# Performance work log

Measured on AMD Instinct MI355X. Metric: run time of the kernel, lower is better.

Reference implementation:

```python
import jax, jax.numpy as jnp
import numpy as np

N = 20000      # total nodes across the mini-batch of graphs
E = 320000     # edges (avg degree 16)
B = 16         # graphs in the batch
HEADS = 8
EPS_BN = 1e-5
NEG_SLOPE = 0.2


def _lin(k, fan_in, fan_out):
    return (jax.random.normal(k, (fan_in, fan_out), jnp.float32) / np.float32(np.sqrt(fan_in)))


def setup_inputs() -> dict:
    key = jax.random.key(0)
    ks = jax.random.split(key, 24)
    inp = {}
    inp["x"] = jax.random.normal(ks[0], (N, 3), jnp.float32)
    inp["edge_index"] = jax.random.randint(ks[1], (2, E), 0, N, dtype=jnp.int32)
    inp["batch"] = jnp.sort(jax.random.randint(ks[2], (N,), 0, B, dtype=jnp.int32))
    # GATConv params: lin weight [in, heads*out], att_src/att_dst [heads,out], bias [heads*out]
    dims = [(3, 16), (128, 32), (256, 64)]
    for i, (cin, cout) in enumerate(dims, start=1):
        base = 3 + 5 * i
        inp[f"W{i}"] = _lin(ks[base], cin, HEADS * cout)
        inp[f"as{i}"] = jax.random.normal(ks[base + 1], (HEADS, cout), jnp.float32) * 0.1
        inp[f"ad{i}"] = jax.random.normal(ks[base + 2], (HEADS, cout), jnp.float32) * 0.1
        inp[f"b{i}"] = jnp.zeros((HEADS * cout,), jnp.float32)
        inp[f"g{i}"] = jnp.ones((HEADS * cout,), jnp.float32)
        inp[f"be{i}"] = jnp.zeros((HEADS * cout,), jnp.float32)
    inp["fcW"] = _lin(ks[20], 512, 10)
    inp["fcb"] = jnp.zeros((10,), jnp.float32)
    return inp


def gat_layer(x, src, dst, W, a_s, a_d, bias, heads, out_ch):
    n = x.shape[0]
    h = (x @ W).reshape(n, heads, out_ch)              # [N,H,C]
    al_s = jnp.einsum('nhc,hc->nh', h, a_s)            # [N,H]
    al_d = jnp.einsum('nhc,hc->nh', h, a_d)
    e = jax.nn.leaky_relu(al_s[src] + al_d[dst], NEG_SLOPE)   # [E,H]
    m = jax.ops.segment_max(e, dst, num_segments=n)    # per-dst softmax (stable)
    e = jnp.exp(e - m[dst])
    denom = jax.ops.segment_sum(e, dst, num_segments=n)
    alpha = e / (denom[dst] + 1e-16)
    out = jax.ops.segment_sum(h[src] * alpha[:, :, None], dst, num_segments=n)
    return out.reshape(n, heads * out_ch) + bias


def bn_relu(x, g, b):
    mu = x.mean(0)
    var = x.var(0)  # biased, as torch BN uses for normalization
    return jax.nn.relu((x - mu) * jax.lax.rsqrt(var + EPS_BN) * g + b)


def reference(x, edge_index, batch, W1, as1, ad1, b1, g1, be1,
              W2, as2, ad2, b2, g2, be2, W3, as3, ad3, b3, g3, be3, fcW, fcb):
    n = x.shape[0]
    loops = jnp.arange(n, dtype=edge_index.dtype)
    src = jnp.concatenate([edge_index[0], loops])  # add_self_loops=True (PyG default)
    dst = jnp.concatenate([edge_index[1], loops])
    h = bn_relu(gat_layer(x, src, dst, W1, as1, ad1, b1, HEADS, 16), g1, be1)
    h = bn_relu(gat_layer(h, src, dst, W2, as2, ad2, b2, HEADS, 32), g2, be2)
    h = bn_relu(gat_layer(h, src, dst, W3, as3, ad3, b3, HEADS, 64), g3, be3)
    pooled = jax.ops.segment_max(h, batch, num_segments=B)  # global_max_pool
    return pooled @ fcW + fcb
```

## Files before the change

kernel.cpp:

```cpp
#include <hip/hip_runtime.h>
#include <hip/hip_bf16.h>

#define HEADS 8
#define EPS_BN 1e-5f
#define NEG_SLOPE 0.2f
#define BN_NB 256

typedef __attribute__((ext_vector_type(8))) short bf16x8;
typedef __attribute__((ext_vector_type(4))) float f32x4;

__device__ __forceinline__ float bf2f(unsigned short u) {
    return __uint_as_float(((unsigned int)u) << 16);
}

__device__ __forceinline__ unsigned short f2bf(float f) {
    __hip_bfloat16 b = __float2bfloat16(f);
    return *reinterpret_cast<unsigned short*>(&b);
}

__device__ __forceinline__ void gld_lds16(const ushort* g, ushort* l) {
    __builtin_amdgcn_global_load_lds(
        (const __attribute__((address_space(1))) unsigned int*)g,
        (__attribute__((address_space(3))) unsigned int*)l, 16, 0, 0);
}


__global__ void count_kernel(const int* __restrict__ ei, int E, int N, int* __restrict__ counts) {
    int i = blockIdx.x * blockDim.x + threadIdx.x;
    int total = E + N;
    if (i >= total) return;
    int d = (i < E) ? ei[E + i] : (i - E);
    atomicAdd(&counts[d], 1);
}

__global__ __launch_bounds__(1024) void scan_block_kernel(const int* __restrict__ counts,
                                                          int* __restrict__ offs,
                                                          int* __restrict__ part, int n) {
    __shared__ int tile[1024];
    int tid = threadIdx.x;
    int gid = blockIdx.x * 1024 + tid;
    int v = (gid < n) ? counts[gid] : 0;
    tile[tid] = v;
    __syncthreads();
    for (int off = 1; off < 1024; off <<= 1) {
        int t = (tid >= off) ? tile[tid - off] : 0;
        __syncthreads();
        tile[tid] += t;
        __syncthreads();
    }
    if (gid < n) offs[gid + 1] = tile[tid];
    if (tid == 1023) part[blockIdx.x] = tile[1023];
}

__global__ __launch_bounds__(1024) void scan_add_kernel(int* __restrict__ offs,
                                                        const int* __restrict__ part, int n) {
    __shared__ int base;
    if (threadIdx.x == 0) {
        int s = 0;
        for (int i = 0; i < (int)blockIdx.x; ++i) s += part[i];
        base = s;
    }
    __syncthreads();
    int gid = blockIdx.x * 1024 + threadIdx.x;
    if (gid < n) offs[gid + 1] += base;
    if (gid == 0) offs[0] = 0;
}

__global__ void scatter_kernel(const int* __restrict__ ei, int E, int N,
                               const int* __restrict__ offs, int* __restrict__ cursor,
                               int* __restrict__ csr_src) {
    int i = blockIdx.x * blockDim.x + threadIdx.x;
    int total = E + N;
    if (i >= total) return;
    int s, d;
    if (i < E) { s = ei[i]; d = ei[E + i]; } else { s = i - E; d = i - E; }
    int slot = atomicAdd(&cursor[d], 1);
    csr_src[offs[d] + slot] = s;
}


__global__ __launch_bounds__(256) void linear1_al_tr_kernel(const float* __restrict__ x,
                                                            const float* __restrict__ W,
                                                            const float* __restrict__ a_s,
                                                            const float* __restrict__ a_d,
                                                            ushort* __restrict__ h,
                                                            float* __restrict__ als,
                                                            float* __restrict__ ald, int N,
                                                            const float* __restrict__ W2,
                                                            ushort* __restrict__ Wt2,
                                                            const float* __restrict__ W3,
                                                            ushort* __restrict__ Wt3) {
    __shared__ float t[32][33];
    int tid = threadIdx.x;
    int bid = blockIdx.x;
    if (bid < 160) {
        const float* Ws; ushort* Wt; int K, Nc, b;
        if (bid < 32) { Ws = W2; Wt = Wt2; K = 128; Nc = 256; b = bid; }
        else          { Ws = W3; Wt = Wt3; K = 256; Nc = 512; b = bid - 32; }
        int nb = Nc / 32;
        int bx = b % nb, by = b / nb;
        int n0 = bx * 32, k0 = by * 32;
        int lx = tid & 31, ly = tid >> 5;
        for (int r = ly; r < 32; r += 8) t[r][lx] = Ws[(size_t)(k0 + r) * Nc + n0 + lx];
        __syncthreads();
        for (int r = ly; r < 32; r += 8) Wt[(size_t)(n0 + r) * K + k0 + lx] = f2bf(t[lx][r]);
    }
    int n = bid * 2 + (tid >> 7);
    int f = tid & 127;
    if (n >= N) return;
    float acc = x[n * 3 + 0] * W[f] + x[n * 3 + 1] * W[128 + f] + x[n * 3 + 2] * W[256 + f];
    h[(size_t)n * 128 + f] = f2bf(acc);
    float s = acc * a_s[f];
    float ds = acc * a_d[f];
    s += __shfl_xor(s, 1);  ds += __shfl_xor(ds, 1);
    s += __shfl_xor(s, 2);  ds += __shfl_xor(ds, 2);
    s += __shfl_xor(s, 4);  ds += __shfl_xor(ds, 4);
    s += __shfl_xor(s, 8);  ds += __shfl_xor(ds, 8);
    if ((f & 15) == 0) {
        int head = f >> 4;
        als[n * 8 + head] = s;
        ald[n * 8 + head] = ds;
    }
}


template<int K, int C>
__global__ __launch_bounds__(256) void mfma_gemm_kernel(const ushort* __restrict__ A,
                                                        const float* __restrict__ scale,
                                                        const float* __restrict__ shift,
                                                        const ushort* __restrict__ Bt,
                                                        ushort* __restrict__ Cout,
                                                        const float* __restrict__ a_s,
                                                        const float* __restrict__ a_d,
                                                        float* __restrict__ als,
                                                        float* __restrict__ ald,
                                                        int M, int Ncols) {
    __shared__ __align__(16) ushort lA[128 * 64];
    __shared__ __align__(16) ushort lB[128 * 64];
    __shared__ __align__(16) float s_scale[K];
    __shared__ __align__(16) float s_shift[K];
    int tid = threadIdx.x;
    int l = tid & 63, w = tid >> 6;
    int m0 = blockIdx.x * 128;
    int n0 = blockIdx.y * 128;
    int wm = w >> 1, wn = w & 1;
    for (int i = tid; i < K; i += 256) {
        s_scale[i] = scale[i];
        s_shift[i] = shift[i];
    }
    f32x4 zero = {0.f, 0.f, 0.f, 0.f};
    f32x4 acc[4][4];
#pragma unroll
    for (int m = 0; m < 4; ++m)
#pragma unroll
        for (int n = 0; n < 4; ++n) acc[m][n] = zero;
    __syncthreads();

#pragma unroll
    for (int k0 = 0; k0 < K; k0 += 64) {
        if (k0) __syncthreads();
#pragma unroll
        for (int i = 0; i < 4; ++i) {
            int idx = (w * 4 + i) * 64 + l;
            int row = idx >> 3, p = idx & 7;
            int gc = (p ^ (row & 7)) * 8;
            gld_lds16(Bt + (size_t)(n0 + row) * K + k0 + gc, &lB[idx * 8]);
        }
#pragma unroll
        for (int i = 0; i < 4; ++i) {
            int idx = (w * 4 + i) * 64 + l;
            int row = idx >> 3, p = idx & 7;
            int gc = (p ^ (row & 7)) * 8;
            int ar = m0 + row; ar = (ar < M) ? ar : (M - 1);
            int kk = k0 + gc;
            uint4 raw = *(const uint4*)(A + (size_t)ar * K + kk);
            float4 sc0 = *(const float4*)(s_scale + kk);
            float4 sc1 = *(const float4*)(s_scale + kk + 4);
            float4 sh0 = *(const float4*)(s_shift + kk);
            float4 sh1 = *(const float4*)(s_shift + kk + 4);
            unsigned int rr0 = raw.x, rr1 = raw.y, rr2 = raw.z, rr3 = raw.w;
            float v0, v1;
            unsigned int o0, o1, o2, o3;
            v0 = fmaxf(__uint_as_float(rr0 << 16) * sc0.x + sh0.x, 0.f);
            v1 = fmaxf(__uint_as_float(rr0 & 0xffff0000u) * sc0.y + sh0.y, 0.f);
            o0 = (unsigned int)f2bf(v0) | ((unsigned int)f2bf(v1) << 16);
            v0 = fmaxf(__uint_as_float(rr1 << 16) * sc0.z + sh0.z, 0.f);
            v1 = fmaxf(__uint_as_float(rr1 & 0xffff0000u) * sc0.w + sh0.w, 0.f);
            o1 = (unsigned int)f2bf(v0) | ((unsigned int)f2bf(v1) << 16);
            v0 = fmaxf(__uint_as_float(rr2 << 16) * sc1.x + sh1.x, 0.f);
            v1 = fmaxf(__uint_as_float(rr2 & 0xffff0000u) * sc1.y + sh1.y, 0.f);
            o2 = (unsigned int)f2bf(v0) | ((unsigned int)f2bf(v1) << 16);
            v0 = fmaxf(__uint_as_float(rr3 << 16) * sc1.z + sh1.z, 0.f);
            v1 = fmaxf(__uint_as_float(rr3 & 0xffff0000u) * sc1.w + sh1.w, 0.f);
            o3 = (unsigned int)f2bf(v0) | ((unsigned int)f2bf(v1) << 16);
            uint4 pk = {o0, o1, o2, o3};
            *(uint4*)&lA[idx * 8] = pk;
        }
        __syncthreads();
#pragma unroll
        for (int ks = 0; ks < 2; ++ks) {
            bf16x8 af[4], bfr[4];
#pragma unroll
            for (int m = 0; m < 4; ++m) {
                int row = wm * 64 + m * 16 + (l & 15);
                int cp = (ks * 4 + (l >> 4)) ^ (row & 7);
                af[m] = *(const bf16x8*)&lA[row * 64 + cp * 8];
            }
#pragma unroll
            for (int n = 0; n < 4; ++n) {
                int row = wn * 64 + n * 16 + (l & 15);
                int cp = (ks * 4 + (l >> 4)) ^ (row & 7);
                bfr[n] = *(const bf16x8*)&lB[row * 64 + cp * 8];
            }
#pragma unroll
            for (int m = 0; m < 4; ++m)
#pragma unroll
                for (int n = 0; n < 4; ++n)
                    acc[m][n] = __builtin_amdgcn_mfma_f32_16x16x32_bf16(af[m], bfr[n], acc[m][n], 0, 0, 0);
        }
    }
    int lr = (l >> 4) * 4, lc = l & 15;
#pragma unroll
    for (int m = 0; m < 4; ++m) {
#pragma unroll
        for (int q = 0; q < 4; ++q) {
            int r = m0 + wm * 64 + m * 16 + lr + q;
            if (r < M) {
#pragma unroll
                for (int n = 0; n < 4; ++n) {
                    int c = n0 + wn * 64 + n * 16 + lc;
                    Cout[(size_t)r * Ncols + c] = f2bf(acc[m][n][q]);
                }
            }
        }
    }
    constexpr int GRP = (C == 64) ? 4 : 2;
    constexpr int NGRP = 4 / GRP;
    float asv[4], adv[4];
#pragma unroll
    for (int n = 0; n < 4; ++n) {
        int cc = n0 + wn * 64 + n * 16 + lc;
        asv[n] = a_s[cc];
        adv[n] = a_d[cc];
    }
#pragma unroll
    for (int m = 0; m < 4; ++m) {
#pragma unroll
        for (int q = 0; q < 4; ++q) {
            int r = m0 + wm * 64 + m * 16 + lr + q;
#pragma unroll
            for (int gg = 0; gg < NGRP; ++gg) {
                float s = 0.f, ds = 0.f;
#pragma unroll
                for (int nn = 0; nn < GRP; ++nn) {
                    int n = gg * GRP + nn;
                    s += acc[m][n][q] * asv[n];
                    ds += acc[m][n][q] * adv[n];
                }
                s += __shfl_xor(s, 1);  ds += __shfl_xor(ds, 1);
                s += __shfl_xor(s, 2);  ds += __shfl_xor(ds, 2);
                s += __shfl_xor(s, 4);  ds += __shfl_xor(ds, 4);
                s += __shfl_xor(s, 8);  ds += __shfl_xor(ds, 8);
                if (lc == 0 && r < M) {
                    int head = (n0 + wn * 64 + gg * (GRP * 16)) / C;
                    als[r * 8 + head] = s;
                    ald[r * 8 + head] = ds;
                }
            }
        }
    }
}


template<int CPL>
__device__ __forceinline__ void gather_accum(const ushort* hp, float wt, float* acc) {
    unsigned int u[CPL / 2];
    if constexpr (CPL == 8) {
        uint4 v = *(const uint4*)hp; u[0] = v.x; u[1] = v.y; u[2] = v.z; u[3] = v.w;
    } else if constexpr (CPL == 4) {
        uint2 v = *(const uint2*)hp; u[0] = v.x; u[1] = v.y;
    } else {
        u[0] = *(const unsigned int*)hp;
    }
#pragma unroll
    for (int j = 0; j < CPL / 2; ++j) {
        acc[2 * j]     += wt * __uint_as_float(u[j] << 16);
        acc[2 * j + 1] += wt * __uint_as_float(u[j] & 0xffff0000u);
    }
}

template<int F, int C>
__global__ __launch_bounds__(256) void aggregate_kernel(const ushort* __restrict__ h,
                                                        const float* __restrict__ als,
                                                        const float* __restrict__ ald,
                                                        const int* __restrict__ offs,
                                                        const int* __restrict__ csr_src,
                                                        const float* __restrict__ bias,
                                                        ushort* __restrict__ outbf, int N) {
    constexpr int CPL = F / 64;
    int w = threadIdx.x >> 6, l = threadIdx.x & 63;
    int d = blockIdx.x * 4 + w;
    if (d >= N) return;
    int start = offs[d];
    int deg = offs[d + 1] - start;
    int hf = l >> 3;
    int hw = l & 7;
    int jslot = l >> 3;
    float aldw = ald[d * 8 + hw];

    float acc[CPL];
#pragma unroll
    for (int j = 0; j < CPL; ++j) acc[j] = 0.f;
    float dsum = 0.f;
    float mrun = -1e30f;

    int nfull = deg & ~7;
    for (int eb = 0; eb < nfull; eb += 8) {
        int sE = (l < 8) ? csr_src[start + eb + l] : 0;
        int smy = __shfl(sE, jslot);
        float v = als[smy * 8 + hw] + aldw;
        v = (v > 0.f) ? v : NEG_SLOPE * v;
        float bm = v;
        bm = fmaxf(bm, __shfl_xor(bm, 8));
        bm = fmaxf(bm, __shfl_xor(bm, 16));
        bm = fmaxf(bm, __shfl_xor(bm, 32));
        float mnew = fmaxf(mrun, bm);
        float rs = __expf(mrun - mnew);
        float pw = __expf(v - mnew);
        dsum = dsum * rs + pw;
        float rsg = __shfl(rs, hf);
#pragma unroll
        for (int j = 0; j < CPL; ++j) acc[j] *= rsg;
        mrun = mnew;
#pragma unroll
        for (int j = 0; j < 8; ++j) {
            int sj = __shfl(sE, j);
            float wt = __shfl(pw, (j << 3) + hf);
            gather_accum<CPL>(h + (size_t)sj * F + l * CPL, wt, acc);
        }
    }
    int rem = deg - nfull;
    if (rem) {
        int sE = (l < rem) ? csr_src[start + nfull + l] : 0;
        int smy = __shfl(sE, jslot);
        float v = -1e30f;
        if (jslot < rem) {
            v = als[smy * 8 + hw] + aldw;
            v = (v > 0.f) ? v : NEG_SLOPE * v;
        }
        float bm = v;
        bm = fmaxf(bm, __shfl_xor(bm, 8));
        bm = fmaxf(bm, __shfl_xor(bm, 16));
        bm = fmaxf(bm, __shfl_xor(bm, 32));
        float mnew = fmaxf(mrun, bm);
        float rs = __expf(mrun - mnew);
        float pw = __expf(v - mnew);
        dsum = dsum * rs + pw;
        float rsg = __shfl(rs, hf);
#pragma unroll
        for (int j = 0; j < CPL; ++j) acc[j] *= rsg;
        for (int j = 0; j < rem; ++j) {
            int sj = __shfl(sE, j);
            float wt = __shfl(pw, (j << 3) + hf);
            gather_accum<CPL>(h + (size_t)sj * F + l * CPL, wt, acc);
        }
    }
    dsum += __shfl_xor(dsum, 8);
    dsum += __shfl_xor(dsum, 16);
    dsum += __shfl_xor(dsum, 32);
    float den = __shfl(dsum, hf);
    float inv = 1.0f / (den + 1e-16f);
    int cbase = l * CPL;
#pragma unroll
    for (int j = 0; j < CPL; ++j)
        outbf[(size_t)d * F + cbase + j] = f2bf(acc[j] * inv + bias[cbase + j]);
}


template<int F>
__global__ __launch_bounds__(256) void bnA_kernel(const ushort* __restrict__ xb,
                                                  float* __restrict__ part,
                                                  int N, int npb) {
    constexpr int F4 = F / 4;
    constexpr int RPI = 256 / F4;
    __shared__ float sdata[256 * 8];
    int tid = threadIdx.x;
    int c4 = tid % F4;
    int ro = tid / F4;
    int n0 = blockIdx.x * npb;
    int n1 = n0 + npb;
    if (n1 > N) n1 = N;
    float s0 = 0, s1 = 0, s2 = 0, s3 = 0, q0 = 0, q1 = 0, q2 = 0, q3 = 0;
    for (int r = n0 + ro; r < n1; r += RPI) {
        ushort4 u = *(const ushort4*)(xb + (size_t)r * F + c4 * 4);
        float v0 = bf2f(u.x), v1 = bf2f(u.y), v2 = bf2f(u.z), v3 = bf2f(u.w);
        s0 += v0; s1 += v1; s2 += v2; s3 += v3;
        q0 += v0 * v0; q1 += v1 * v1; q2 += v2 * v2; q3 += v3 * v3;
    }
    float* sp = &sdata[tid * 8];
    sp[0] = s0; sp[1] = s1; sp[2] = s2; sp[3] = s3;
    sp[4] = q0; sp[5] = q1; sp[6] = q2; sp[7] = q3;
    __syncthreads();
    if (tid < F4) {
        float t[8];
#pragma unroll
        for (int k = 0; k < 8; ++k) t[k] = sdata[tid * 8 + k];
        for (int j = 1; j < RPI; ++j) {
            const float* op = &sdata[(j * F4 + tid) * 8];
#pragma unroll
            for (int k = 0; k < 8; ++k) t[k] += op[k];
        }
        float* pb = part + (size_t)blockIdx.x * 2 * F;
#pragma unroll
        for (int k = 0; k < 4; ++k) {
            pb[tid * 4 + k]     = t[k];
            pb[F + tid * 4 + k] = t[4 + k];
        }
    }
}

template<int F>
__global__ void bnB_kernel(const float* __restrict__ part,
                           const float* __restrict__ g, const float* __restrict__ be,
                           float* __restrict__ scale, float* __restrict__ shift, int N) {
    int f = blockIdx.x * blockDim.x + threadIdx.x;
    if (f >= F) return;
    float sum = 0.f, sq = 0.f;
#pragma unroll 4
    for (int j = 0; j < BN_NB; ++j) {
        sum += part[(size_t)j * 2 * F + f];
        sq  += part[(size_t)j * 2 * F + F + f];
    }
    float invN = 1.0f / (float)N;
    float mean = sum * invN;
    float var = sq * invN - mean * mean;
    float sc = g[f] * rsqrtf(var + EPS_BN);
    scale[f] = sc;
    shift[f] = be[f] - mean * sc;
}


__global__ __launch_bounds__(256) void poolA_kernel(const ushort* __restrict__ xb,
                                                    const int* __restrict__ batch,
                                                    const float* __restrict__ scale,
                                                    const float* __restrict__ shift,
                                                    float* __restrict__ pooled8, int N) {
    int tid = threadIdx.x;
    int c4 = tid & 127;
    int ro = tid >> 7;
    int n0 = blockIdx.x * 64;
    int n1 = n0 + 64;
    if (n1 > N) n1 = N;
    float4 sc = ((const float4*)scale)[c4];
    float4 sh = ((const float4*)shift)[c4];
    float* pbase = pooled8 + (size_t)(blockIdx.x & 7) * (16 * 512);
    float m0 = 0.f, m1 = 0.f, m2 = 0.f, m3 = 0.f;
    int cur = -1;
    for (int n = n0 + ro; n < n1; n += 2) {
        int b = batch[n];
        if (b != cur) {
            if (cur >= 0) {
                int base = cur * 512 + c4 * 4;
                atomicMax((int*)&pbase[base],     __float_as_int(m0));
                atomicMax((int*)&pbase[base + 1], __float_as_int(m1));
                atomicMax((int*)&pbase[base + 2], __float_as_int(m2));
                atomicMax((int*)&pbase[base + 3], __float_as_int(m3));
            }
            cur = b;
            m0 = m1 = m2 = m3 = 0.f;
        }
        ushort4 u = *(const ushort4*)(xb + (size_t)n * 512 + c4 * 4);
        m0 = fmaxf(m0, bf2f(u.x) * sc.x + sh.x);
        m1 = fmaxf(m1, bf2f(u.y) * sc.y + sh.y);
        m2 = fmaxf(m2, bf2f(u.z) * sc.z + sh.z);
        m3 = fmaxf(m3, bf2f(u.w) * sc.w + sh.w);
    }
    if (cur >= 0) {
        int base = cur * 512 + c4 * 4;
        atomicMax((int*)&pbase[base],     __float_as_int(m0));
        atomicMax((int*)&pbase[base + 1], __float_as_int(m1));
        atomicMax((int*)&pbase[base + 2], __float_as_int(m2));
        atomicMax((int*)&pbase[base + 3], __float_as_int(m3));
    }
}

__global__ __launch_bounds__(512) void poolFC_kernel(const float* __restrict__ pooled8,
                                                     const float* __restrict__ fcW,
                                                     const float* __restrict__ fcb,
                                                     float* __restrict__ out) {
    __shared__ float sp[16 * 513];
    __shared__ float sw[512 * 10];
    int tid = threadIdx.x;
    for (int c = tid; c < 16 * 512; c += 512) {
        float m = pooled8[c];
#pragma unroll
        for (int k = 1; k < 8; ++k) m = fmaxf(m, pooled8[k * 16 * 512 + c]);
        int b = c >> 9, f = c & 511;
        sp[b * 513 + f] = m;
    }
    for (int i = tid; i < 512 * 10; i += 512) sw[i] = fcW[i];
    __syncthreads();
    if (tid < 160) {
        int b = tid / 10, j = tid % 10;
        float acc = fcb[j];
        const float* spb = &sp[b * 513];
#pragma unroll 8
        for (int f = 0; f < 512; ++f) acc += spb[f] * sw[f * 10 + j];
        out[tid] = acc;
    }
}


extern "C" void kernel_launch(void* const* d_in, const int* in_sizes, int n_in,
                              void* d_out, int out_size, void* d_ws, size_t ws_size,
                              hipStream_t stream) {
    const float* x   = (const float*)d_in[0];
    const int* ei    = (const int*)d_in[1];
    const int* batch = (const int*)d_in[2];
    const float* W1  = (const float*)d_in[3];
    const float* as1 = (const float*)d_in[4];
    const float* ad1 = (const float*)d_in[5];
    const float* b1  = (const float*)d_in[6];
    const float* g1  = (const float*)d_in[7];
    const float* be1 = (const float*)d_in[8];
    const float* W2  = (const float*)d_in[9];
    const float* as2 = (const float*)d_in[10];
    const float* ad2 = (const float*)d_in[11];
    const float* b2  = (const float*)d_in[12];
    const float* g2  = (const float*)d_in[13];
    const float* be2 = (const float*)d_in[14];
    const float* W3  = (const float*)d_in[15];
    const float* as3 = (const float*)d_in[16];
    const float* ad3 = (const float*)d_in[17];
    const float* b3  = (const float*)d_in[18];
    const float* g3  = (const float*)d_in[19];
    const float* be3 = (const float*)d_in[20];
    const float* fcW = (const float*)d_in[21];
    const float* fcb = (const float*)d_in[22];
    float* out = (float*)d_out;

    int N = in_sizes[0] / 3;
    int E = in_sizes[1] / 2;

    char* p = (char*)d_ws;
    auto alloc = [&](size_t bytes) {
        char* r = p;
        p += (bytes + 255) & ~(size_t)255;
        return r;
    };
    char* zbase   = p;
    int*   counts = (int*)alloc((size_t)N * 4);
    int*   cursor = (int*)alloc((size_t)N * 4);
    float* pooled8 = (float*)alloc(8 * 16 * 512 * 4);
    size_t zbytes = (size_t)(p - zbase);
    int*   offs   = (int*)alloc((size_t)(N + 1) * 4);
    int*   part   = (int*)alloc(64 * 4);
    int*   csr    = (int*)alloc((size_t)(E + N) * 4);
    ushort* h     = (ushort*)alloc((size_t)N * 512 * 2);
    ushort* aggbf = (ushort*)alloc((size_t)N * 512 * 2);
    ushort* Wt2   = (ushort*)alloc(256 * 128 * 2);
    ushort* Wt3   = (ushort*)alloc(512 * 256 * 2);
    float* als    = (float*)alloc((size_t)N * 8 * 4);
    float* ald    = (float*)alloc((size_t)N * 8 * 4);
    float* bnpart = (float*)alloc((size_t)BN_NB * 1024 * 4);
    float* scale  = (float*)alloc(512 * 4);
    float* shift  = (float*)alloc(512 * 4);

    int total_e = E + N;
    int nchunks = (N + 1023) / 1024;
    int mtiles = (N + 127) / 128;
    int bnnpb = (N + BN_NB - 1) / BN_NB;
    int ablocks = (N + 3) / 4;
    int pblocks = (N + 63) / 64;

    hipMemsetAsync(zbase, 0, zbytes, stream);

    count_kernel<<<(total_e + 255) / 256, 256, 0, stream>>>(ei, E, N, counts);
    scan_block_kernel<<<nchunks, 1024, 0, stream>>>(counts, offs, part, N);
    scan_add_kernel<<<nchunks, 1024, 0, stream>>>(offs, part, N);
    scatter_kernel<<<(total_e + 255) / 256, 256, 0, stream>>>(ei, E, N, offs, cursor, csr);

    linear1_al_tr_kernel<<<(N + 1) / 2, 256, 0, stream>>>(x, W1, as1, ad1, h, als, ald, N,
                                                          W2, Wt2, W3, Wt3);
    aggregate_kernel<128, 16><<<ablocks, 256, 0, stream>>>(h, als, ald, offs, csr, b1, aggbf, N);
    bnA_kernel<128><<<BN_NB, 256, 0, stream>>>(aggbf, bnpart, N, bnnpb);
    bnB_kernel<128><<<1, 128, 0, stream>>>(bnpart, g1, be1, scale, shift, N);

    mfma_gemm_kernel<128, 32><<<dim3(mtiles, 2), 256, 0, stream>>>(
        aggbf, scale, shift, Wt2, h, as2, ad2, als, ald, N, 256);
    aggregate_kernel<256, 32><<<ablocks, 256, 0, stream>>>(h, als, ald, offs, csr, b2, aggbf, N);
    bnA_kernel<256><<<BN_NB, 256, 0, stream>>>(aggbf, bnpart, N, bnnpb);
    bnB_kernel<256><<<1, 256, 0, stream>>>(bnpart, g2, be2, scale, shift, N);

    mfma_gemm_kernel<256, 64><<<dim3(mtiles, 4), 256, 0, stream>>>(
        aggbf, scale, shift, Wt3, h, as3, ad3, als, ald, N, 512);
    aggregate_kernel<512, 64><<<ablocks, 256, 0, stream>>>(h, als, ald, offs, csr, b3, aggbf, N);
    bnA_kernel<512><<<BN_NB, 256, 0, stream>>>(aggbf, bnpart, N, bnnpb);
    bnB_kernel<512><<<2, 256, 0, stream>>>(bnpart, g3, be3, scale, shift, N);

    poolA_kernel<<<pblocks, 256, 0, stream>>>(aggbf, batch, scale, shift, pooled8, N);
    poolFC_kernel<<<1, 512, 0, stream>>>(pooled8, fcW, fcb, out);
}
```

Measured before the change: 318.6 us.

## Fuse BN statistics into GAT aggregation epilogue and parallelize BN finalize

The separate bnA pass that re-read the aggregated bf16 features is removed. Its per-feature sum and sum-of-squares are now accumulated in shared memory inside the aggregate kernel, which grows to 8 warps per block, and written out as per-block partials. bnB is rewritten to reduce the roughly 2500 partials across several blocks, each using 8 row-groups. This saves a full read of the activations per layer, but adds LDS atomics in the epilogue and a much larger partial buffer that bnB must read.

Measured after the change: 658.0 us. 107% more time.

```diff
diff --git a/kernel.cpp b/kernel.cpp
--- a/kernel.cpp
+++ b/kernel.cpp
@@ -4,7 +4,6 @@
 #define HEADS 8
 #define EPS_BN 1e-5f
 #define NEG_SLOPE 0.2f
-#define BN_NB 256
 
 typedef __attribute__((ext_vector_type(8))) short bf16x8;
 typedef __attribute__((ext_vector_type(4))) float f32x4;
@@ -290,153 +289,142 @@
 }
 
 template<int F, int C>
-__global__ __launch_bounds__(256) void aggregate_kernel(const ushort* __restrict__ h,
+__global__ __launch_bounds__(512) void aggregate_kernel(const ushort* __restrict__ h,
                                                         const float* __restrict__ als,
                                                         const float* __restrict__ ald,
                                                         const int* __restrict__ offs,
                                                         const int* __restrict__ csr_src,
                                                         const float* __restrict__ bias,
-                                                        ushort* __restrict__ outbf, int N) {
+                                                        ushort* __restrict__ outbf,
+                                                        float* __restrict__ bnpart, int N) {
     constexpr int CPL = F / 64;
-    int w = threadIdx.x >> 6, l = threadIdx.x & 63;
-    int d = blockIdx.x * 4 + w;
-    if (d >= N) return;
-    int start = offs[d];
-    int deg = offs[d + 1] - start;
-    int hf = l >> 3;
-    int hw = l & 7;
-    int jslot = l >> 3;
-    float aldw = ald[d * 8 + hw];
-
-    float acc[CPL];
-#pragma unroll
-    for (int j = 0; j < CPL; ++j) acc[j] = 0.f;
-    float dsum = 0.f;
-    float mrun = -1e30f;
-
-    int nfull = deg & ~7;
-    for (int eb = 0; eb < nfull; eb += 8) {
-        int sE = (l < 8) ? csr_src[start + eb + l] : 0;
-        int smy = __shfl(sE, jslot);
-        float v = als[smy * 8 + hw] + aldw;
-        v = (v > 0.f) ? v : NEG_SLOPE * v;
-        float bm = v;
-        bm = fmaxf(bm, __shfl_xor(bm, 8));
-        bm = fmaxf(bm, __shfl_xor(bm, 16));
-        bm = fmaxf(bm, __shfl_xor(bm, 32));
-        float mnew = fmaxf(mrun, bm);
-        float rs = __expf(mrun - mnew);
-        float pw = __expf(v - mnew);
-        dsum = dsum * rs + pw;
-        float rsg = __shfl(rs, hf);
-#pragma unroll
-        for (int j = 0; j < CPL; ++j) acc[j] *= rsg;
-        mrun = mnew;
-#pragma unroll
-        for (int j = 0; j < 8; ++j) {
-            int sj = __shfl(sE, j);
-            float wt = __shfl(pw, (j << 3) + hf);
-            gather_accum<CPL>(h + (size_t)sj * F + l * CPL, wt, acc);
-        }
-    }
-    int rem = deg - nfull;
-    if (rem) {
-        int sE = (l < rem) ? csr_src[start + nfull + l] : 0;
-        int smy = __shfl(sE, jslot);
-        float v = -1e30f;
-        if (jslot < rem) {
-            v = als[smy * 8 + hw] + aldw;
+    __shared__ float sstat[2 * F];
+    int tid = threadIdx.x;
+    int w = tid >> 6, l = tid & 63;
+    int d = blockIdx.x * 8 + w;
+    for (int i = tid; i < 2 * F; i += 512) sstat[i] = 0.f;
+    __syncthreads();
+
+    if (d < N) {
+        int start = offs[d];
+        int deg = offs[d + 1] - start;
+        int hf = l >> 3;
+        int hw = l & 7;
+        int jslot = l >> 3;
+        float aldw = ald[d * 8 + hw];
+
+        float acc[CPL];
+#pragma unroll
+        for (int j = 0; j < CPL; ++j) acc[j] = 0.f;
+        float dsum = 0.f;
+        float mrun = -1e30f;
+
+        int nfull = deg & ~7;
+        for (int eb = 0; eb < nfull; eb += 8) {
+            int sE = (l < 8) ? csr_src[start + eb + l] : 0;
+            int smy = __shfl(sE, jslot);
+            float v = als[smy * 8 + hw] + aldw;
             v = (v > 0.f) ? v : NEG_SLOPE * v;
-        }
-        float bm = v;
-        bm = fmaxf(bm, __shfl_xor(bm, 8));
-        bm = fmaxf(bm, __shfl_xor(bm, 16));
-        bm = fmaxf(bm, __shfl_xor(bm, 32));
-        float mnew = fmaxf(mrun, bm);
-        float rs = __expf(mrun - mnew);
-        float pw = __expf(v - mnew);
-        dsum = dsum * rs + pw;
-        float rsg = __shfl(rs, hf);
-#pragma unroll
-        for (int j = 0; j < CPL; ++j) acc[j] *= rsg;
-        for (int j = 0; j < rem; ++j) {
-            int sj = __shfl(sE, j);
-            float wt = __shfl(pw, (j << 3) + hf);
-            gather_accum<CPL>(h + (size_t)sj * F + l * CPL, wt, acc);
-        }
-    }
-    dsum += __shfl_xor(dsum, 8);
-    dsum += __shfl_xor(dsum, 16);
-    dsum += __shfl_xor(dsum, 32);
-    float den = __shfl(dsum, hf);
-    float inv = 1.0f / (den + 1e-16f);
-    int cbase = l * CPL;
-#pragma unroll
-    for (int j = 0; j < CPL; ++j)
-        outbf[(size_t)d * F + cbase + j] = f2bf(acc[j] * inv + bias[cbase + j]);
+            float bm = v;
+            bm = fmaxf(bm, __shfl_xor(bm, 8));
+            bm = fmaxf(bm, __shfl_xor(bm, 16));
+            bm = fmaxf(bm, __shfl_xor(bm, 32));
+            float mnew = fmaxf(mrun, bm);
+            float rs = __expf(mrun - mnew);
+            float pw = __expf(v - mnew);
+            dsum = dsum * rs + pw;
+            float rsg = __shfl(rs, hf);
+#pragma unroll
+            for (int j = 0; j < CPL; ++j) acc[j] *= rsg;
+            mrun = mnew;
+#pragma unroll
+            for (int j = 0; j < 8; ++j) {
+                int sj = __shfl(sE, j);
+                float wt = __shfl(pw, (j << 3) + hf);
+                gather_accum<CPL>(h + (size_t)sj * F + l * CPL, wt, acc);
+            }
+        }
+        int rem = deg - nfull;
+        if (rem) {
+            int sE = (l < rem) ? csr_src[start + nfull + l] : 0;
+            int smy = __shfl(sE, jslot);
+            float v = -1e30f;
+            if (jslot < rem) {
+                v = als[smy * 8 + hw] + aldw;
+                v = (v > 0.f) ? v : NEG_SLOPE * v;
+            }
+            float bm = v;
+            bm = fmaxf(bm, __shfl_xor(bm, 8));
+            bm = fmaxf(bm, __shfl_xor(bm, 16));
+            bm = fmaxf(bm, __shfl_xor(bm, 32));
+            float mnew = fmaxf(mrun, bm);
+            float rs = __expf(mrun - mnew);
+            float pw = __expf(v - mnew);
+            dsum = dsum * rs + pw;
+            float rsg = __shfl(rs, hf);
+#pragma unroll
+            for (int j = 0; j < CPL; ++j) acc[j] *= rsg;
+            for (int j = 0; j < rem; ++j) {
+                int sj = __shfl(sE, j);
+                float wt = __shfl(pw, (j << 3) + hf);
+                gather_accum<CPL>(h + (size_t)sj * F + l * CPL, wt, acc);
+            }
+        }
+        dsum += __shfl_xor(dsum, 8);
+        dsum += __shfl_xor(dsum, 16);
+        dsum += __shfl_xor(dsum, 32);
+        float den = __shfl(dsum, hf);
+        float inv = 1.0f / (den + 1e-16f);
+        int cbase = l * CPL;
+#pragma unroll
+        for (int j = 0; j < CPL; ++j) {
+            unsigned short ob = f2bf(acc[j] * inv + bias[cbase + j]);
+            outbf[(size_t)d * F + cbase + j] = ob;
+            float vv = bf2f(ob);
+            atomicAdd(&sstat[cbase + j], vv);
+            atomicAdd(&sstat[F + cbase + j], vv * vv);
+        }
+    }
+    __syncthreads();
+    float* pb = bnpart + (size_t)blockIdx.x * 2 * F;
+    for (int i = tid; i < 2 * F; i += 512) pb[i] = sstat[i];
 }
 
 
 template<int F>
-__global__ __launch_bounds__(256) void bnA_kernel(const ushort* __restrict__ xb,
-                                                  float* __restrict__ part,
-                                                  int N, int npb) {
-    constexpr int F4 = F / 4;
-    constexpr int RPI = 256 / F4;
-    __shared__ float sdata[256 * 8];
-    int tid = threadIdx.x;
-    int c4 = tid % F4;
-    int ro = tid / F4;
-    int n0 = blockIdx.x * npb;
-    int n1 = n0 + npb;
-    if (n1 > N) n1 = N;
-    float s0 = 0, s1 = 0, s2 = 0, s3 = 0, q0 = 0, q1 = 0, q2 = 0, q3 = 0;
-    for (int r = n0 + ro; r < n1; r += RPI) {
-        ushort4 u = *(const ushort4*)(xb + (size_t)r * F + c4 * 4);
-        float v0 = bf2f(u.x), v1 = bf2f(u.y), v2 = bf2f(u.z), v3 = bf2f(u.w);
-        s0 += v0; s1 += v1; s2 += v2; s3 += v3;
-        q0 += v0 * v0; q1 += v1 * v1; q2 += v2 * v2; q3 += v3 * v3;
-    }
-    float* sp = &sdata[tid * 8];
-    sp[0] = s0; sp[1] = s1; sp[2] = s2; sp[3] = s3;
-    sp[4] = q0; sp[5] = q1; sp[6] = q2; sp[7] = q3;
-    __syncthreads();
-    if (tid < F4) {
-        float t[8];
-#pragma unroll
-        for (int k = 0; k < 8; ++k) t[k] = sdata[tid * 8 + k];
-        for (int j = 1; j < RPI; ++j) {
-            const float* op = &sdata[(j * F4 + tid) * 8];
-#pragma unroll
-            for (int k = 0; k < 8; ++k) t[k] += op[k];
-        }
-        float* pb = part + (size_t)blockIdx.x * 2 * F;
-#pragma unroll
-        for (int k = 0; k < 4; ++k) {
-            pb[tid * 4 + k]     = t[k];
-            pb[F + tid * 4 + k] = t[4 + k];
-        }
-    }
-}
-
-template<int F>
-__global__ void bnB_kernel(const float* __restrict__ part,
-                           const float* __restrict__ g, const float* __restrict__ be,
-                           float* __restrict__ scale, float* __restrict__ shift, int N) {
-    int f = blockIdx.x * blockDim.x + threadIdx.x;
-    if (f >= F) return;
-    float sum = 0.f, sq = 0.f;
-#pragma unroll 4
-    for (int j = 0; j < BN_NB; ++j) {
-        sum += part[(size_t)j * 2 * F + f];
-        sq  += part[(size_t)j * 2 * F + F + f];
-    }
-    float invN = 1.0f / (float)N;
-    float mean = sum * invN;
-    float var = sq * invN - mean * mean;
-    float sc = g[f] * rsqrtf(var + EPS_BN);
-    scale[f] = sc;
-    shift[f] = be[f] - mean * sc;
+__global__ __launch_bounds__(256) void bnB_kernel(const float* __restrict__ part,
+                                                  const float* __restrict__ g,
+                                                  const float* __restrict__ be,
+                                                  float* __restrict__ scale,
+                                                  float* __restrict__ shift,
+                                                  int N, int nb) {
+    __shared__ float sd[8][2][33];
+    int fl = threadIdx.x & 31;
+    int bc = threadIdx.x >> 5;
+    int f = blockIdx.x * 32 + fl;
+    int per = (nb + 7) / 8;
+    int b0 = bc * per;
+    int b1 = b0 + per; if (b1 > nb) b1 = nb;
+    float s = 0.f, q = 0.f;
+    for (int b = b0; b < b1; ++b) {
+        s += part[(size_t)b * 2 * F + f];
+        q += part[(size_t)b * 2 * F + F + f];
+    }
+    sd[bc][0][fl] = s;
+    sd[bc][1][fl] = q;
+    __syncthreads();
+    if (threadIdx.x < 32) {
+        float ss = 0.f, qq = 0.f;
+#pragma unroll
+        for (int k = 0; k < 8; ++k) { ss += sd[k][0][threadIdx.x]; qq += sd[k][1][threadIdx.x]; }
+        int fo = blockIdx.x * 32 + threadIdx.x;
+        float invN = 1.0f / (float)N;
+        float mean = ss * invN;
+        float var = qq * invN - mean * mean;
+        float sc = g[fo] * rsqrtf(var + EPS_BN);
+        scale[fo] = sc;
+        shift[fo] = be[fo] - mean * sc;
+    }
 }
 
 
@@ -562,15 +550,14 @@
     ushort* Wt3   = (ushort*)alloc(512 * 256 * 2);
     float* als    = (float*)alloc((size_t)N * 8 * 4);
     float* ald    = (float*)alloc((size_t)N * 8 * 4);
-    float* bnpart = (float*)alloc((size_t)BN_NB * 1024 * 4);
+    int ablocks   = (N + 7) / 8;
+    float* bnpart = (float*)alloc((size_t)ablocks * 2 * 512 * 4);
     float* scale  = (float*)alloc(512 * 4);
     float* shift  = (float*)alloc(512 * 4);
 
     int total_e = E + N;
     int nchunks = (N + 1023) / 1024;
     int mtiles = (N + 127) / 128;
-    int bnnpb = (N + BN_NB - 1) / BN_NB;
-    int ablocks = (N + 3) / 4;
     int pblocks = (N + 63) / 64;
 
     hipMemsetAsync(zbase, 0, zbytes, stream);
@@ -582,21 +569,21 @@
 
     linear1_al_tr_kernel<<<(N + 1) / 2, 256, 0, stream>>>(x, W1, as1, ad1, h, als, ald, N,
                                                           W2, Wt2, W3, Wt3);
-    aggregate_kernel<128, 16><<<ablocks, 256, 0, stream>>>(h, als, ald, offs, csr, b1, aggbf, N);
-    bnA_kernel<128><<<BN_NB, 256, 0, stream>>>(aggbf, bnpart, N, bnnpb);
-    bnB_kernel<128><<<1, 128, 0, stream>>>(bnpart, g1, be1, scale, shift, N);
+    aggregate_kernel<128, 16><<<ablocks, 512, 0, stream>>>(h, als, ald, offs, csr, b1,
+                                                           aggbf, bnpart, N);
+    bnB_kernel<128><<<4, 256, 0, stream>>>(bnpart, g1, be1, scale, shift, N, ablocks);
 
     mfma_gemm_kernel<128, 32><<<dim3(mtiles, 2), 256, 0, stream>>>(
         aggbf, scale, shift, Wt2, h, as2, ad2, als, ald, N, 256);
-    aggregate_kernel<256, 32><<<ablocks, 256, 0, stream>>>(h, als, ald, offs, csr, b2, aggbf, N);
-    bnA_kernel<256><<<BN_NB, 256, 0, stream>>>(aggbf, bnpart, N, bnnpb);
-    bnB_kernel<256><<<1, 256, 0, stream>>>(bnpart, g2, be2, scale, shift, N);
+    aggregate_kernel<256, 32><<<ablocks, 512, 0, stream>>>(h, als, ald, offs, csr, b2,
+                                                           aggbf, bnpart, N);
+    bnB_kernel<256><<<8, 256, 0, stream>>>(bnpart, g2, be2, scale, shift, N, ablocks);
 
     mfma_gemm_kernel<256, 64><<<dim3(mtiles, 4), 256, 0, stream>>>(
         aggbf, scale, shift, Wt3, h, as3, ad3, als, ald, N, 512);
-    aggregate_kernel<512, 64><<<ablocks, 256, 0, stream>>>(h, als, ald, offs, csr, b3, aggbf, N);
-    bnA_kernel<512><<<BN_NB, 256, 0, stream>>>(aggbf, bnpart, N, bnnpb);
-    bnB_kernel<512><<<2, 256, 0, stream>>>(bnpart, g3, be3, scale, shift, N);
+    aggregate_kernel<512, 64><<<ablocks, 512, 0, stream>>>(h, als, ald, offs, csr, b3,
+                                                           aggbf, bnpart, N);
+    bnB_kernel<512><<<16, 256, 0, stream>>>(bnpart, g3, be3, scale, shift, N, ablocks);
 
     poolA_kernel<<<pblocks, 256, 0, stream>>>(aggbf, batch, scale, shift, pooled8, N);
     poolFC_kernel<<<1, 512, 0, stream>>>(pooled8, fcW, fcb, out);
```
